# Performance work log

Measured on AMD Instinct MI355X. Metric: run time of the kernel, lower is better.

Reference implementation:

```python
import jax, jax.numpy as jnp
import numpy as np

B, S, H = 64, 1024, 1000

def setup_inputs() -> dict:
    key = jax.random.key(0)
    k1, k2, k3, k4 = jax.random.split(key, 4)
    h_tgt = jax.random.normal(k1, (B, 1, H), dtype=jnp.float32)
    h_src = jax.random.normal(k2, (B, S, H), dtype=jnp.float32)
    # nn.Linear(H, H) params: weight [H, H], bias [H]
    bound = 1.0 / np.sqrt(H)
    W = jax.random.uniform(k3, (H, H), dtype=jnp.float32, minval=-bound, maxval=bound)
    b = jax.random.uniform(k4, (H,), dtype=jnp.float32, minval=-bound, maxval=bound)
    return {"h_tgt": h_tgt, "h_src": h_src, "W": W, "b": b}

def reference(h_tgt, h_src, W, b):
    # score[b,t] = h_tgt[b,0] . (W @ h_src[b,t] + bias)  -- Luong general attention
    proj = jnp.einsum('bsh,gh->bsg', h_src, W) + b          # [B,S,H]
    score = jnp.einsum('bh,bsh->bs', h_tgt[:, 0], proj)      # [B,S]
    a = jax.nn.softmax(score, axis=1)                        # [B,S]
    c = jnp.einsum('bs,bsh->bh', a, h_src)[:, None, :]       # [B,1,H]
    return c
```

## Files before the change

kernel.cpp:

```cpp
#include <hip/hip_runtime.h>

typedef float v4f __attribute__((ext_vector_type(4)));
typedef float v2f __attribute__((ext_vector_type(2)));

constexpr int Bb = 64;
constexpr int Ss = 1024;
constexpr int Hh = 1000;
constexpr int CHUNKS = 32;
constexpr int CS = Ss / CHUNKS;
constexpr int BG = 4;
constexpr int PW = 8;
constexpr int GL = Hh / PW;

__global__ __launch_bounds__(512) void proj_tgt_kernel(
    const float* __restrict__ h_tgt, const float* __restrict__ W,
    float* __restrict__ u)
{
    const int tid  = (int)threadIdx.x;
    const int lane = tid & 63;
    const int w    = tid >> 6;
    const int b0   = (int)blockIdx.x * BG;
    const int slot = (int)blockIdx.y * 64 + lane;
    const bool ok  = (slot < Hh / 2);
    const int h    = slot * 2;

    v2f acc[BG];
    #pragma unroll
    for (int bi = 0; bi < BG; ++bi) acc[bi] = (v2f){0.f, 0.f};

    const int gbase = w * GL;
    const float* wp = W + (size_t)gbase * Hh + h;
    #pragma unroll 4
    for (int g = 0; g < GL; ++g) {
        const v2f w2 = ok ? *(const v2f*)wp : (v2f){0.f, 0.f};
        #pragma unroll
        for (int bi = 0; bi < BG; ++bi) {
            const float a = h_tgt[(b0 + bi) * Hh + gbase + g];
            acc[bi] += a * w2;
        }
        wp += Hh;
    }

    __shared__ v2f red[BG][PW][64];
    #pragma unroll
    for (int bi = 0; bi < BG; ++bi) red[bi][w][lane] = acc[bi];
    __syncthreads();

    if (w < BG) {
        v2f s = red[w][0][lane];
        #pragma unroll
        for (int p = 1; p < PW; ++p) s += red[w][p][lane];
        if (ok) *(v2f*)(u + (size_t)(b0 + w) * Hh + h) = s;
    }
}

__global__ __launch_bounds__(256) void attn_partial_kernel(
    const float* __restrict__ h_src, const float* __restrict__ u,
    float* __restrict__ wsM, float* __restrict__ wsL, float* __restrict__ wsC)
{
    const int lane  = threadIdx.x & 63;
    const int wave  = (int)((blockIdx.x * blockDim.x + threadIdx.x) >> 6);
    const int b     = wave >> 5;
    const int chunk = wave & 31;
    const int s0    = chunk * CS;

    const float* ub = u + b * Hh;
    v4f uf[4];
    #pragma unroll
    for (int j = 0; j < 4; ++j) {
        const int d = j * 256 + lane * 4;
        uf[j] = (d < Hh) ? *(const v4f*)(ub + d) : (v4f){0.f, 0.f, 0.f, 0.f};
    }

    float m = -INFINITY, l = 0.f;
    v4f c[4];
    #pragma unroll
    for (int j = 0; j < 4; ++j) c[j] = (v4f){0.f, 0.f, 0.f, 0.f};

    const float* xp = h_src + (size_t)(b * Ss + s0) * Hh;
    for (int s = 0; s < CS; s += 4) {
        v4f x[4][4];
        #pragma unroll
        for (int r = 0; r < 4; ++r) {
            #pragma unroll
            for (int j = 0; j < 4; ++j) {
                const int d = j * 256 + lane * 4;
                x[r][j] = (d < Hh)
                    ? __builtin_nontemporal_load((const v4f*)(xp + (size_t)r * Hh + d))
                    : (v4f){0.f, 0.f, 0.f, 0.f};
            }
        }
        float p[4] = {0.f, 0.f, 0.f, 0.f};
        #pragma unroll
        for (int r = 0; r < 4; ++r) {
            #pragma unroll
            for (int j = 0; j < 4; ++j) {
                p[r] = fmaf(x[r][j].x, uf[j].x, p[r]);
                p[r] = fmaf(x[r][j].y, uf[j].y, p[r]);
                p[r] = fmaf(x[r][j].z, uf[j].z, p[r]);
                p[r] = fmaf(x[r][j].w, uf[j].w, p[r]);
            }
        }
        #pragma unroll
        for (int off = 32; off > 0; off >>= 1) {
            #pragma unroll
            for (int r = 0; r < 4; ++r) p[r] += __shfl_xor(p[r], off, 64);
        }

        const float mx01 = fmaxf(p[0], p[1]);
        const float mx23 = fmaxf(p[2], p[3]);
        const float mn = fmaxf(m, fmaxf(mx01, mx23));
        if (mn > m) {
            const float scale = __expf(m - mn);
            m = mn;
            l *= scale;
            #pragma unroll
            for (int j = 0; j < 4; ++j) c[j] *= scale;
        }
        float e[4];
        #pragma unroll
        for (int r = 0; r < 4; ++r) e[r] = __expf(p[r] - m);
        l += (e[0] + e[1]) + (e[2] + e[3]);
        #pragma unroll
        for (int r = 0; r < 4; ++r) {
            #pragma unroll
            for (int j = 0; j < 4; ++j) {
                c[j].x = fmaf(e[r], x[r][j].x, c[j].x);
                c[j].y = fmaf(e[r], x[r][j].y, c[j].y);
                c[j].z = fmaf(e[r], x[r][j].z, c[j].z);
                c[j].w = fmaf(e[r], x[r][j].w, c[j].w);
            }
        }
        xp += 4 * Hh;
    }

    const int idx = b * CHUNKS + chunk;
    if (lane == 0) { wsM[idx] = m; wsL[idx] = l; }
    float* cw = wsC + (size_t)idx * Hh;
    #pragma unroll
    for (int j = 0; j < 4; ++j) {
        const int d = j * 256 + lane * 4;
        if (d < Hh) *(v4f*)(cw + d) = c[j];
    }
}

__global__ __launch_bounds__(128) void combine_kernel(
    const float* __restrict__ wsM, const float* __restrict__ wsL,
    const float* __restrict__ wsC, float* __restrict__ out)
{
    const int b    = (int)blockIdx.x;
    const int half = (int)blockIdx.y;
    const int tid  = (int)threadIdx.x;
    __shared__ float sw[CHUNKS];
    __shared__ float sInvL;

    if (tid < 64) {
        const bool v = (tid < CHUNKS);
        const float mi = v ? wsM[b * CHUNKS + tid] : -INFINITY;
        const float li = v ? wsL[b * CHUNKS + tid] : 0.f;
        float M = mi;
        #pragma unroll
        for (int off = 32; off > 0; off >>= 1) M = fmaxf(M, __shfl_xor(M, off, 64));
        const float w = __expf(mi - M);
        float L = w * li;
        #pragma unroll
        for (int off = 32; off > 0; off >>= 1) L += __shfl_xor(L, off, 64);
        if (v) sw[tid] = w;
        if (tid == 0) sInvL = 1.f / L;
    }
    __syncthreads();

    const int slot = half * 125 + tid;
    if (tid < 125) {
        const int h = slot * 4;
        v4f acc = (v4f){0.f, 0.f, 0.f, 0.f};
        #pragma unroll 8
        for (int i = 0; i < CHUNKS; ++i)
            acc += sw[i] * *(const v4f*)(wsC + (size_t)(b * CHUNKS + i) * Hh + h);
        *(v4f*)(out + b * Hh + h) = acc * sInvL;
    }
}

extern "C" void kernel_launch(void* const* d_in, const int* in_sizes, int n_in,
                              void* d_out, int out_size, void* d_ws, size_t ws_size,
                              hipStream_t stream) {
    const float* h_tgt = (const float*)d_in[0];
    const float* h_src = (const float*)d_in[1];
    const float* W     = (const float*)d_in[2];
    float* out = (float*)d_out;

    float* u   = (float*)d_ws;
    float* wsM = u + Bb * Hh;
    float* wsL = wsM + Bb * CHUNKS;
    float* wsC = wsL + Bb * CHUNKS;

    proj_tgt_kernel<<<dim3(Bb / BG, 8), 512, 0, stream>>>(h_tgt, W, u);
    attn_partial_kernel<<<(Bb * CHUNKS) / 4, 256, 0, stream>>>(h_src, u, wsM, wsL, wsC);
    combine_kernel<<<dim3(Bb, 2), 128, 0, stream>>>(wsM, wsL, wsC, out);
}
```

Measured before the change: 373.2 us.

## Fuse combine into attention kernel via last-block atomic counter; stage h_tgt in LDS

Removes the separate combine kernel launch by having the last block to finish for each batch (detected with a per-batch atomic counter and threadfences) perform the softmax merge and output write. Counters are zeroed inside the projection kernel. The projection kernel now stages its four h_tgt rows in shared memory and unrolls the W loop further. This saves one launch and its gap but adds fences and atomics, and the tail combine now runs serially at the end of a few blocks.

```diff
diff --git a/kernel.cpp b/kernel.cpp
--- a/kernel.cpp
+++ b/kernel.cpp
@@ -11,10 +11,11 @@
 constexpr int BG = 4;
 constexpr int PW = 8;
 constexpr int GL = Hh / PW;
+constexpr int BLK_PER_B = CHUNKS / 4;
 
 __global__ __launch_bounds__(512) void proj_tgt_kernel(
     const float* __restrict__ h_tgt, const float* __restrict__ W,
-    float* __restrict__ u)
+    float* __restrict__ u, int* __restrict__ counters)
 {
     const int tid  = (int)threadIdx.x;
     const int lane = tid & 63;
@@ -24,22 +25,27 @@
     const bool ok  = (slot < Hh / 2);
     const int h    = slot * 2;
 
+    if (blockIdx.x == 0 && blockIdx.y == 0 && tid < Bb) counters[tid] = 0;
+
+    __shared__ float sA[BG * Hh];
+    for (int i = tid; i < BG * Hh; i += 512) sA[i] = h_tgt[b0 * Hh + i];
+    __syncthreads();
+
     v2f acc[BG];
     #pragma unroll
     for (int bi = 0; bi < BG; ++bi) acc[bi] = (v2f){0.f, 0.f};
 
     const int gbase = w * GL;
     const float* wp = W + (size_t)gbase * Hh + h;
-    #pragma unroll 4
+    #pragma unroll 8
     for (int g = 0; g < GL; ++g) {
         const v2f w2 = ok ? *(const v2f*)wp : (v2f){0.f, 0.f};
         #pragma unroll
-        for (int bi = 0; bi < BG; ++bi) {
-            const float a = h_tgt[(b0 + bi) * Hh + gbase + g];
-            acc[bi] += a * w2;
-        }
+        for (int bi = 0; bi < BG; ++bi)
+            acc[bi] += sA[bi * Hh + gbase + g] * w2;
         wp += Hh;
     }
+    __syncthreads();
 
     __shared__ v2f red[BG][PW][64];
     #pragma unroll
@@ -54,9 +60,10 @@
     }
 }
 
-__global__ __launch_bounds__(256) void attn_partial_kernel(
+__global__ __launch_bounds__(256) void attn_kernel(
     const float* __restrict__ h_src, const float* __restrict__ u,
-    float* __restrict__ wsM, float* __restrict__ wsL, float* __restrict__ wsC)
+    float* __restrict__ wsM, float* __restrict__ wsL, float* __restrict__ wsC,
+    int* __restrict__ counters, float* __restrict__ out)
 {
     const int lane  = threadIdx.x & 63;
     const int wave  = (int)((blockIdx.x * blockDim.x + threadIdx.x) >> 6);
@@ -142,18 +149,21 @@
         const int d = j * 256 + lane * 4;
         if (d < Hh) *(v4f*)(cw + d) = c[j];
     }
-}
-
-__global__ __launch_bounds__(128) void combine_kernel(
-    const float* __restrict__ wsM, const float* __restrict__ wsL,
-    const float* __restrict__ wsC, float* __restrict__ out)
-{
-    const int b    = (int)blockIdx.x;
-    const int half = (int)blockIdx.y;
-    const int tid  = (int)threadIdx.x;
+
+    __threadfence();
+    __syncthreads();
+    __shared__ int sLast;
+    if (threadIdx.x == 0) {
+        const int prev = atomicAdd(&counters[b], 1);
+        sLast = (prev == BLK_PER_B - 1);
+    }
+    __syncthreads();
+    if (!sLast) return;
+    __threadfence();
+
     __shared__ float sw[CHUNKS];
     __shared__ float sInvL;
-
+    const int tid = (int)threadIdx.x;
     if (tid < 64) {
         const bool v = (tid < CHUNKS);
         const float mi = v ? wsM[b * CHUNKS + tid] : -INFINITY;
@@ -161,18 +171,17 @@
         float M = mi;
         #pragma unroll
         for (int off = 32; off > 0; off >>= 1) M = fmaxf(M, __shfl_xor(M, off, 64));
-        const float w = __expf(mi - M);
-        float L = w * li;
+        const float w2 = __expf(mi - M);
+        float L = w2 * li;
         #pragma unroll
         for (int off = 32; off > 0; off >>= 1) L += __shfl_xor(L, off, 64);
-        if (v) sw[tid] = w;
+        if (v) sw[tid] = w2;
         if (tid == 0) sInvL = 1.f / L;
     }
     __syncthreads();
 
-    const int slot = half * 125 + tid;
-    if (tid < 125) {
-        const int h = slot * 4;
+    if (tid < 250) {
+        const int h = tid * 4;
         v4f acc = (v4f){0.f, 0.f, 0.f, 0.f};
         #pragma unroll 8
         for (int i = 0; i < CHUNKS; ++i)
@@ -193,8 +202,8 @@
     float* wsM = u + Bb * Hh;
     float* wsL = wsM + Bb * CHUNKS;
     float* wsC = wsL + Bb * CHUNKS;
-
-    proj_tgt_kernel<<<dim3(Bb / BG, 8), 512, 0, stream>>>(h_tgt, W, u);
-    attn_partial_kernel<<<(Bb * CHUNKS) / 4, 256, 0, stream>>>(h_src, u, wsM, wsL, wsC);
-    combine_kernel<<<dim3(Bb, 2), 128, 0, stream>>>(wsM, wsL, wsC, out);
+    int*   ctr = (int*)(wsC + (size_t)Bb * CHUNKS * Hh);
+
+    proj_tgt_kernel<<<dim3(Bb / BG, 8), 512, 0, stream>>>(h_tgt, W, u, ctr);
+    attn_kernel<<<(Bb * CHUNKS) / 4, 256, 0, stream>>>(h_src, u, wsM, wsL, wsC, ctr, out);
 }
```

Measured after the change: 489.8 us. +31.2%, slower.
